# Performance work log

Hardware: AMD Instinct MI355X
Metric: run time of the kernel (lower is better)

Reference implementation:

```python
import jax, jax.numpy as jnp
import numpy as np

N_NODES = 100000
N_EDGES = 1600000


def gcn_conv(x, edge_index, W, b):
    # PyG GCNConv: add self-loops, symmetric degree normalization,
    # linear transform, scatter-sum aggregation, + bias.
    n = x.shape[0]
    loop = jnp.arange(n, dtype=edge_index.dtype)
    src = jnp.concatenate([edge_index[0], loop])
    dst = jnp.concatenate([edge_index[1], loop])
    deg = jnp.zeros((n,), x.dtype).at[dst].add(1.0)
    dinv = jnp.where(deg > 0, deg ** -0.5, 0.0)
    norm = dinv[src] * dinv[dst]            # [E+N]
    h = x @ W                               # [N, out]
    msg = h[src] * norm[:, None]            # gather + scale
    out = jax.ops.segment_sum(msg, dst, num_segments=n)
    return out + b


def setup_inputs() -> dict:
    key = jax.random.key(0)
    k1, k2, k3, k4 = jax.random.split(key, 4)
    d_in, d_lat, d_out = 512, 128, 64
    x = jax.random.normal(k1, (N_NODES, d_in), jnp.float32)
    edge_index = jax.random.randint(k2, (2, N_EDGES), 0, N_NODES, jnp.int64)
    W1 = jax.random.normal(k3, (d_in, d_lat), jnp.float32) * (d_in ** -0.5)
    b1 = jnp.zeros((d_lat,), jnp.float32)
    W2 = jax.random.normal(k4, (d_lat, d_out), jnp.float32) * (d_lat ** -0.5)
    b2 = jnp.zeros((d_out,), jnp.float32)
    return {"x": x, "edge_index": edge_index, "W1": W1, "b1": b1, "W2": W2, "b2": b2}


def reference(x, edge_index, W1, b1, W2, b2):
    h = gcn_conv(x, edge_index, W1, b1)
    h = gcn_conv(h, edge_index, W2, b2)
    return jax.nn.relu(h)
```

## Files before the change

kernel.cpp:

```cpp
#include <hip/hip_runtime.h>
#include <hip/hip_bf16.h>

typedef unsigned short u16;
typedef unsigned int   u32;

#define N_NODES 100000
#define N_EDGES 1600000

__device__ __forceinline__ float bf2f(u16 u) {
    union { u32 i; float f; } c; c.i = ((u32)u) << 16; return c.f;
}
__device__ __forceinline__ u16 f2bf(float f) {
    union { float f; u32 i; } c; c.f = f;
    u32 u = c.i;
    u += 0x7fffu + ((u >> 16) & 1u);
    return (u16)(u >> 16);
}

__global__ void k_detect(const u32* __restrict__ ei, int* __restrict__ flag) {
    if (threadIdx.x == 0 && blockIdx.x == 0) {
        u32 h = ei[1] | ei[3] | ei[5] | ei[7];
        *flag = (h == 0u) ? 1 : 0;
    }
}
__device__ __forceinline__ int edge_at(const u32* ei, int f, long pos) {
    return f ? (int)ei[2 * pos] : (int)ei[pos];
}


__global__ void k_degree(const u32* __restrict__ ei, const int* __restrict__ flag,
                         int* __restrict__ deg) {
    int e = blockIdx.x * blockDim.x + threadIdx.x;
    int f = *flag;
    if (e < N_EDGES) atomicAdd(&deg[edge_at(ei, f, (long)N_EDGES + e)], 1);
}

__global__ void k_scan_part(const int* __restrict__ deg, int* __restrict__ rowstart,
                            int* __restrict__ bsums) {
    __shared__ int sh[256];
    const int t = threadIdx.x, b = blockIdx.x;
    const int base = b * 2048 + t * 8;
    int v[8]; int s = 0;
#pragma unroll
    for (int i = 0; i < 8; i++) {
        int idx = base + i;
        v[i] = (idx < N_NODES) ? deg[idx] : 0;
        s += v[i];
    }
    sh[t] = s;
    __syncthreads();
    for (int d = 1; d < 256; d <<= 1) {
        int x = (t >= d) ? sh[t - d] : 0;
        __syncthreads();
        sh[t] += x;
        __syncthreads();
    }
    int acc = sh[t] - s;
#pragma unroll
    for (int i = 0; i < 8; i++) {
        int idx = base + i;
        if (idx < N_NODES) rowstart[idx] = acc;
        acc += v[i];
    }
    if (t == 255) bsums[b] = sh[255];
}

__global__ void k_scan_sums(const int* __restrict__ bsums, int* __restrict__ boffs, int nb) {
    if (threadIdx.x == 0 && blockIdx.x == 0) {
        int r = 0;
        for (int i = 0; i < nb; i++) { boffs[i] = r; r += bsums[i]; }
    }
}

__global__ void k_scan_add_dinv(int* __restrict__ rowstart, const int* __restrict__ boffs,
                                const int* __restrict__ deg, float* __restrict__ dinv) {
    int i = blockIdx.x * blockDim.x + threadIdx.x;
    if (i < N_NODES) {
        rowstart[i] += boffs[i >> 11];
        dinv[i] = rsqrtf((float)(deg[i] + 1));
    }
    if (i == 0) rowstart[N_NODES] = N_EDGES;
}

__global__ void k_fill(const u32* __restrict__ ei, const int* __restrict__ flag,
                       const int* __restrict__ rowstart, int* __restrict__ cursor,
                       int* __restrict__ csr) {
    int e = blockIdx.x * blockDim.x + threadIdx.x;
    int f = *flag;
    if (e < N_EDGES) {
        int s = edge_at(ei, f, e);
        int d = edge_at(ei, f, (long)N_EDGES + e);
        int p = rowstart[d] + atomicAdd(&cursor[d], 1);
        csr[p] = s;
    }
}


__global__ void k_w12(const float* __restrict__ W1, const float* __restrict__ W2,
                      float* __restrict__ W12f) {
    int idx = blockIdx.x * 256 + threadIdx.x;
    int k = idx >> 6, n = idx & 63;
    float acc = 0.f;
#pragma unroll 4
    for (int j = 0; j < 128; j++) acc += W1[k * 128 + j] * W2[j * 64 + n];
    W12f[idx] = acc;
}

__global__ void k_c1(const float* __restrict__ b1, const float* __restrict__ W2,
                     float* __restrict__ c1) {
    int n = threadIdx.x;
    float acc = 0.f;
    for (int j = 0; j < 128; j++) acc += b1[j] * W2[j * 64 + n];
    c1[n] = acc;
}

__global__ void k_fragB(const float* __restrict__ W12f, u16* __restrict__ Bt) {
    int idx = blockIdx.x * 256 + threadIdx.x;
    int l = idx & 63, c = (idx >> 6) & 3, kt = idx >> 8;
    int n = c * 16 + (l & 15);
    int k0 = kt * 32 + (l >> 4) * 8;
    u32 p[4];
#pragma unroll
    for (int j = 0; j < 4; j++) {
        u16 a = f2bf(W12f[(k0 + 2 * j) * 64 + n]);
        u16 b = f2bf(W12f[(k0 + 2 * j + 1) * 64 + n]);
        p[j] = (u32)a | ((u32)b << 16);
    }
    *(uint4*)&Bt[(long)idx * 8] = make_uint4(p[0], p[1], p[2], p[3]);
}


__global__ __launch_bounds__(256) void gemm_x(const float* __restrict__ A,
                                              const u16* __restrict__ Bt,
                                              u16* __restrict__ C, int M) {
    constexpr int SA = 40;
    __shared__ u16 As[128 * SA];
    typedef __attribute__((ext_vector_type(8))) short v8s;
    typedef __attribute__((ext_vector_type(4))) float v4f;

    const int t = threadIdx.x;
    const int wave = t >> 6, lane = t & 63;
    const int m = lane & 15, quad = lane >> 4;
    const int row0 = blockIdx.x * 128;

    v4f acc[2][4];
#pragma unroll
    for (int i = 0; i < 2; i++)
#pragma unroll
        for (int c = 0; c < 4; c++)
#pragma unroll
            for (int r = 0; r < 4; r++) acc[i][c][r] = 0.0f;

    const int arow = t >> 1, ahalf = t & 1;
    const long aoff = (long)(row0 + arow) * 512;
    const bool arow_ok = (row0 + arow) < M;

    for (int kt = 0; kt < 16; ++kt) {
        const int kk0 = kt * 32 + ahalf * 16;
        float4 f0 = make_float4(0.f, 0.f, 0.f, 0.f), f1 = f0, f2 = f0, f3 = f0;
        if (arow_ok) {
            f0 = *(const float4*)&A[aoff + kk0];
            f1 = *(const float4*)&A[aoff + kk0 + 4];
            f2 = *(const float4*)&A[aoff + kk0 + 8];
            f3 = *(const float4*)&A[aoff + kk0 + 12];
        }
        uint4 w0, w1;
        w0.x = (u32)f2bf(f0.x) | ((u32)f2bf(f0.y) << 16);
        w0.y = (u32)f2bf(f0.z) | ((u32)f2bf(f0.w) << 16);
        w0.z = (u32)f2bf(f1.x) | ((u32)f2bf(f1.y) << 16);
        w0.w = (u32)f2bf(f1.z) | ((u32)f2bf(f1.w) << 16);
        w1.x = (u32)f2bf(f2.x) | ((u32)f2bf(f2.y) << 16);
        w1.y = (u32)f2bf(f2.z) | ((u32)f2bf(f2.w) << 16);
        w1.z = (u32)f2bf(f3.x) | ((u32)f2bf(f3.y) << 16);
        w1.w = (u32)f2bf(f3.z) | ((u32)f2bf(f3.w) << 16);
        *(uint4*)&As[arow * SA + ahalf * 16] = w0;
        *(uint4*)&As[arow * SA + ahalf * 16 + 8] = w1;
        __syncthreads();
        v8s a0 = *(const v8s*)&As[(wave * 32 + m) * SA + quad * 8];
        v8s a1 = *(const v8s*)&As[(wave * 32 + 16 + m) * SA + quad * 8];
#pragma unroll
        for (int c = 0; c < 4; c++) {
            v8s b = *(const v8s*)&Bt[(long)((kt * 4 + c) * 64 + lane) * 8];
            acc[0][c] = __builtin_amdgcn_mfma_f32_16x16x32_bf16(a0, b, acc[0][c], 0, 0, 0);
            acc[1][c] = __builtin_amdgcn_mfma_f32_16x16x32_bf16(a1, b, acc[1][c], 0, 0, 0);
        }
        __syncthreads();
    }
#pragma unroll
    for (int i = 0; i < 2; i++)
#pragma unroll
        for (int c = 0; c < 4; c++)
#pragma unroll
            for (int r = 0; r < 4; r++) {
                int grow = row0 + wave * 32 + i * 16 + quad * 4 + r;
                if (grow < M) C[(long)grow * 64 + c * 16 + m] = f2bf(acc[i][c][r]);
            }
}


__global__ __launch_bounds__(256) void agg_a(const u16* __restrict__ z,
                                             const float* __restrict__ dinv,
                                             const int* __restrict__ rowstart,
                                             const int* __restrict__ csr,
                                             u16* __restrict__ y) {
    const int wave = threadIdx.x >> 6, lane = threadIdx.x & 63;
    const int n = blockIdx.x * 4 + wave;
    const int half = lane >> 5, l = lane & 31;
    const u32* z32 = (const u32*)z;
    float a0 = 0.f, a1 = 0.f;
    const float w0 = dinv[n];
    if (half == 0) {
        u32 d = z32[(long)n * 32 + l];
        float w = w0 * w0;
        a0 += bf2f((u16)(d & 0xffffu)) * w;
        a1 += bf2f((u16)(d >> 16)) * w;
    }
    const int i1 = rowstart[n + 1];
    for (int i = rowstart[n] + half; i < i1; i += 2) {
        int s = csr[i];
        float w = dinv[s] * w0;
        u32 d = z32[(long)s * 32 + l];
        a0 += bf2f((u16)(d & 0xffffu)) * w;
        a1 += bf2f((u16)(d >> 16)) * w;
    }
    a0 += __shfl_down(a0, 32);
    a1 += __shfl_down(a1, 32);
    if (half == 0) {
        u32 o = (u32)f2bf(a0) | ((u32)f2bf(a1) << 16);
        ((u32*)y)[(long)n * 32 + l] = o;
    }
}


__global__ __launch_bounds__(256) void agg_b(const u16* __restrict__ y,
                                             const float* __restrict__ dinv,
                                             const int* __restrict__ rowstart,
                                             const int* __restrict__ csr,
                                             const float* __restrict__ c1,
                                             const float* __restrict__ b2,
                                             float* __restrict__ out) {
    const int wave = threadIdx.x >> 6, lane = threadIdx.x & 63;
    const int n = blockIdx.x * 4 + wave;
    const int half = lane >> 5, l = lane & 31;
    const u32* y32 = (const u32*)y;
    float a0 = 0.f, a1 = 0.f, sacc = 0.f;
    const float w0 = dinv[n];
    if (half == 0) {
        u32 d = y32[(long)n * 32 + l];
        float w = w0 * w0;
        sacc += w;
        a0 += bf2f((u16)(d & 0xffffu)) * w;
        a1 += bf2f((u16)(d >> 16)) * w;
    }
    const int i1 = rowstart[n + 1];
    for (int i = rowstart[n] + half; i < i1; i += 2) {
        int s = csr[i];
        float w = dinv[s] * w0;
        sacc += w;
        u32 d = y32[(long)s * 32 + l];
        a0 += bf2f((u16)(d & 0xffffu)) * w;
        a1 += bf2f((u16)(d >> 16)) * w;
    }
    a0 += __shfl_down(a0, 32);
    a1 += __shfl_down(a1, 32);
    sacc += __shfl_down(sacc, 32);
    if (half == 0) {
        float2 cv = ((const float2*)c1)[l];
        float2 bv = ((const float2*)b2)[l];
        float r0 = fmaxf(a0 + sacc * cv.x + bv.x, 0.f);
        float r1 = fmaxf(a1 + sacc * cv.y + bv.y, 0.f);
        ((float2*)out)[(long)n * 32 + l] = make_float2(r0, r1);
    }
}


extern "C" void kernel_launch(void* const* d_in, const int* in_sizes, int n_in,
                              void* d_out, int out_size, void* d_ws, size_t ws_size,
                              hipStream_t stream) {
    const float* x  = (const float*)d_in[0];
    const u32*   ei = (const u32*)d_in[1];
    const float* W1 = (const float*)d_in[2];
    const float* b1 = (const float*)d_in[3];
    const float* W2 = (const float*)d_in[4];
    const float* b2 = (const float*)d_in[5];
    float* out = (float*)d_out;

    char* ws = (char*)d_ws;
    size_t o = 0;
    auto alloc = [&](size_t bytes) -> char* {
        char* p = ws + o;
        o = (o + bytes + 255) & ~(size_t)255;
        return p;
    };
    int*   deg      = (int*)  alloc(N_NODES * 4);
    float* dinv     = (float*)alloc(N_NODES * 4);
    int*   rowstart = (int*)  alloc((N_NODES + 1) * 4);
    int*   cursor   = (int*)  alloc(N_NODES * 4);
    int*   bsums    = (int*)  alloc(64 * 4);
    int*   boffs    = (int*)  alloc(64 * 4);
    int*   eflag    = (int*)  alloc(256);
    float* W12f     = (float*)alloc(512 * 64 * 4);
    u16*   Bt       = (u16*)  alloc(512 * 64 * 2);
    float* c1       = (float*)alloc(64 * 4);
    int*   csr      = (int*)  alloc((size_t)N_EDGES * 4);
    u16*   z        = (u16*)  alloc((size_t)N_NODES * 64 * 2);
    u16*   y        = (u16*)  alloc((size_t)N_NODES * 64 * 2);
    (void)ws_size;

    hipMemsetAsync(deg, 0, N_NODES * 4, stream);
    hipMemsetAsync(cursor, 0, N_NODES * 4, stream);

    const int EB = (N_EDGES + 255) / 256;
    const int NB = (N_NODES + 255) / 256;
    const int SCAN_BLKS = (N_NODES + 2047) / 2048;

    k_detect<<<1, 64, 0, stream>>>(ei, eflag);
    k_degree<<<EB, 256, 0, stream>>>(ei, eflag, deg);
    k_scan_part<<<SCAN_BLKS, 256, 0, stream>>>(deg, rowstart, bsums);
    k_scan_sums<<<1, 64, 0, stream>>>(bsums, boffs, SCAN_BLKS);
    k_scan_add_dinv<<<NB, 256, 0, stream>>>(rowstart, boffs, deg, dinv);
    k_fill<<<EB, 256, 0, stream>>>(ei, eflag, rowstart, cursor, csr);

    k_w12<<<128, 256, 0, stream>>>(W1, W2, W12f);
    k_c1<<<1, 64, 0, stream>>>(b1, W2, c1);
    k_fragB<<<16, 256, 0, stream>>>(W12f, Bt);

    gemm_x<<<(N_NODES + 127) / 128, 256, 0, stream>>>(x, Bt, z, N_NODES);
    agg_a<<<N_NODES / 4, 256, 0, stream>>>(z, dinv, rowstart, csr, y);
    agg_b<<<N_NODES / 4, 256, 0, stream>>>(y, dinv, rowstart, csr, c1, b2, out);
}
```

Before: 711.0 us.

## Prescale features by dinv, widen aggregation lanes, vectorize CSR build

The GEMM epilogue now multiplies each output row by dinv, so the aggregation loops become plain sums without a per-edge dinv multiply. The source-side normalisation for layer two is folded into a per-node factor (sfac) that agg_a precomputes. Both aggregation kernels now use four 16-lane groups reading 8 bytes each and unroll two edges per iteration, which raises memory-level parallelism. CSR construction handles four edges per thread with vector loads and initialises cursor directly from rowstart, removing a memset and a rowstart lookup. The extra bf16 rounding after prescaling slightly changes numerics.

```diff
diff --git a/kernel.cpp b/kernel.cpp
--- a/kernel.cpp
+++ b/kernel.cpp
@@ -16,6 +16,12 @@
     u += 0x7fffu + ((u >> 16) & 1u);
     return (u16)(u >> 16);
 }
+__device__ __forceinline__ void acc4(uint2 d, float& a0, float& a1, float& a2, float& a3) {
+    a0 += bf2f((u16)(d.x & 0xffffu));
+    a1 += bf2f((u16)(d.x >> 16));
+    a2 += bf2f((u16)(d.y & 0xffffu));
+    a3 += bf2f((u16)(d.y >> 16));
+}
 
 __global__ void k_detect(const u32* __restrict__ ei, int* __restrict__ flag) {
     if (threadIdx.x == 0 && blockIdx.x == 0) {
@@ -30,9 +36,24 @@
 
 __global__ void k_degree(const u32* __restrict__ ei, const int* __restrict__ flag,
                          int* __restrict__ deg) {
-    int e = blockIdx.x * blockDim.x + threadIdx.x;
+    int e4 = blockIdx.x * 256 + threadIdx.x;
     int f = *flag;
-    if (e < N_EDGES) atomicAdd(&deg[edge_at(ei, f, (long)N_EDGES + e)], 1);
+    long e = 4L * e4;
+    if (e + 3 < N_EDGES) {
+        int d0, d1, d2, d3;
+        if (f) {
+            uint4 a = *(const uint4*)&ei[2 * ((long)N_EDGES + e)];
+            uint4 b = *(const uint4*)&ei[2 * ((long)N_EDGES + e) + 4];
+            d0 = (int)a.x; d1 = (int)a.z; d2 = (int)b.x; d3 = (int)b.z;
+        } else {
+            uint4 a = *(const uint4*)&ei[(long)N_EDGES + e];
+            d0 = (int)a.x; d1 = (int)a.y; d2 = (int)a.z; d3 = (int)a.w;
+        }
+        atomicAdd(&deg[d0], 1); atomicAdd(&deg[d1], 1);
+        atomicAdd(&deg[d2], 1); atomicAdd(&deg[d3], 1);
+    } else {
+        for (; e < N_EDGES; e++) atomicAdd(&deg[edge_at(ei, f, (long)N_EDGES + e)], 1);
+    }
 }
 
 __global__ void k_scan_part(const int* __restrict__ deg, int* __restrict__ rowstart,
@@ -73,25 +94,48 @@
 }
 
 __global__ void k_scan_add_dinv(int* __restrict__ rowstart, const int* __restrict__ boffs,
-                                const int* __restrict__ deg, float* __restrict__ dinv) {
+                                const int* __restrict__ deg, float* __restrict__ dinv,
+                                int* __restrict__ cursor) {
     int i = blockIdx.x * blockDim.x + threadIdx.x;
     if (i < N_NODES) {
-        rowstart[i] += boffs[i >> 11];
+        int r = rowstart[i] + boffs[i >> 11];
+        rowstart[i] = r;
+        cursor[i] = r;
         dinv[i] = rsqrtf((float)(deg[i] + 1));
     }
     if (i == 0) rowstart[N_NODES] = N_EDGES;
 }
 
 __global__ void k_fill(const u32* __restrict__ ei, const int* __restrict__ flag,
-                       const int* __restrict__ rowstart, int* __restrict__ cursor,
-                       int* __restrict__ csr) {
-    int e = blockIdx.x * blockDim.x + threadIdx.x;
+                       int* __restrict__ cursor, int* __restrict__ csr) {
+    int e4 = blockIdx.x * 256 + threadIdx.x;
     int f = *flag;
-    if (e < N_EDGES) {
-        int s = edge_at(ei, f, e);
-        int d = edge_at(ei, f, (long)N_EDGES + e);
-        int p = rowstart[d] + atomicAdd(&cursor[d], 1);
-        csr[p] = s;
+    long e = 4L * e4;
+    if (e + 3 < N_EDGES) {
+        int s0, s1, s2, s3, d0, d1, d2, d3;
+        if (f) {
+            uint4 a = *(const uint4*)&ei[2 * e];
+            uint4 b = *(const uint4*)&ei[2 * e + 4];
+            s0 = (int)a.x; s1 = (int)a.z; s2 = (int)b.x; s3 = (int)b.z;
+            uint4 c = *(const uint4*)&ei[2 * ((long)N_EDGES + e)];
+            uint4 d = *(const uint4*)&ei[2 * ((long)N_EDGES + e) + 4];
+            d0 = (int)c.x; d1 = (int)c.z; d2 = (int)d.x; d3 = (int)d.z;
+        } else {
+            uint4 a = *(const uint4*)&ei[e];
+            s0 = (int)a.x; s1 = (int)a.y; s2 = (int)a.z; s3 = (int)a.w;
+            uint4 c = *(const uint4*)&ei[(long)N_EDGES + e];
+            d0 = (int)c.x; d1 = (int)c.y; d2 = (int)c.z; d3 = (int)c.w;
+        }
+        csr[atomicAdd(&cursor[d0], 1)] = s0;
+        csr[atomicAdd(&cursor[d1], 1)] = s1;
+        csr[atomicAdd(&cursor[d2], 1)] = s2;
+        csr[atomicAdd(&cursor[d3], 1)] = s3;
+    } else {
+        for (; e < N_EDGES; e++) {
+            int s = edge_at(ei, f, e);
+            int d = edge_at(ei, f, (long)N_EDGES + e);
+            csr[atomicAdd(&cursor[d], 1)] = s;
+        }
     }
 }
 
@@ -132,6 +176,7 @@
 
 __global__ __launch_bounds__(256) void gemm_x(const float* __restrict__ A,
                                               const u16* __restrict__ Bt,
+                                              const float* __restrict__ dinv,
                                               u16* __restrict__ C, int M) {
     constexpr int SA = 40;
     __shared__ u16 As[128 * SA];
@@ -189,87 +234,112 @@
 #pragma unroll
     for (int i = 0; i < 2; i++)
 #pragma unroll
-        for (int c = 0; c < 4; c++)
-#pragma unroll
-            for (int r = 0; r < 4; r++) {
-                int grow = row0 + wave * 32 + i * 16 + quad * 4 + r;
-                if (grow < M) C[(long)grow * 64 + c * 16 + m] = f2bf(acc[i][c][r]);
+        for (int r = 0; r < 4; r++) {
+            int grow = row0 + wave * 32 + i * 16 + quad * 4 + r;
+            if (grow < M) {
+                float w = dinv[grow];
+#pragma unroll
+                for (int c = 0; c < 4; c++)
+                    C[(long)grow * 64 + c * 16 + m] = f2bf(acc[i][c][r] * w);
             }
-}
-
-
-__global__ __launch_bounds__(256) void agg_a(const u16* __restrict__ z,
+        }
+}
+
+
+__global__ __launch_bounds__(256) void agg_a(const u16* __restrict__ zp,
                                              const float* __restrict__ dinv,
                                              const int* __restrict__ rowstart,
                                              const int* __restrict__ csr,
-                                             u16* __restrict__ y) {
+                                             u16* __restrict__ yp,
+                                             float* __restrict__ sfac) {
     const int wave = threadIdx.x >> 6, lane = threadIdx.x & 63;
     const int n = blockIdx.x * 4 + wave;
-    const int half = lane >> 5, l = lane & 31;
-    const u32* z32 = (const u32*)z;
-    float a0 = 0.f, a1 = 0.f;
+    const int g = lane >> 4, l = lane & 15;
+    const uint2* z2 = (const uint2*)zp;
+    float a0 = 0.f, a1 = 0.f, a2 = 0.f, a3 = 0.f, sd = 0.f;
     const float w0 = dinv[n];
-    if (half == 0) {
-        u32 d = z32[(long)n * 32 + l];
-        float w = w0 * w0;
-        a0 += bf2f((u16)(d & 0xffffu)) * w;
-        a1 += bf2f((u16)(d >> 16)) * w;
+    if (g == 0) {
+        uint2 d = z2[(long)n * 16 + l];
+        acc4(d, a0, a1, a2, a3);
+        sd = w0;
     }
     const int i1 = rowstart[n + 1];
-    for (int i = rowstart[n] + half; i < i1; i += 2) {
+    int i = rowstart[n] + g;
+    for (; i + 4 < i1; i += 8) {
+        int s0 = csr[i], s1 = csr[i + 4];
+        uint2 d0 = z2[(long)s0 * 16 + l];
+        uint2 d1 = z2[(long)s1 * 16 + l];
+        sd += dinv[s0] + dinv[s1];
+        acc4(d0, a0, a1, a2, a3);
+        acc4(d1, a0, a1, a2, a3);
+    }
+    if (i < i1) {
         int s = csr[i];
-        float w = dinv[s] * w0;
-        u32 d = z32[(long)s * 32 + l];
-        a0 += bf2f((u16)(d & 0xffffu)) * w;
-        a1 += bf2f((u16)(d >> 16)) * w;
-    }
-    a0 += __shfl_down(a0, 32);
-    a1 += __shfl_down(a1, 32);
-    if (half == 0) {
-        u32 o = (u32)f2bf(a0) | ((u32)f2bf(a1) << 16);
-        ((u32*)y)[(long)n * 32 + l] = o;
-    }
-}
-
-
-__global__ __launch_bounds__(256) void agg_b(const u16* __restrict__ y,
+        uint2 d = z2[(long)s * 16 + l];
+        sd += dinv[s];
+        acc4(d, a0, a1, a2, a3);
+    }
+    a0 += __shfl_xor(a0, 16); a0 += __shfl_xor(a0, 32);
+    a1 += __shfl_xor(a1, 16); a1 += __shfl_xor(a1, 32);
+    a2 += __shfl_xor(a2, 16); a2 += __shfl_xor(a2, 32);
+    a3 += __shfl_xor(a3, 16); a3 += __shfl_xor(a3, 32);
+    sd += __shfl_xor(sd, 16); sd += __shfl_xor(sd, 32);
+    if (g == 0) {
+        float w2 = w0 * w0;
+        uint2 o;
+        o.x = (u32)f2bf(a0 * w2) | ((u32)f2bf(a1 * w2) << 16);
+        o.y = (u32)f2bf(a2 * w2) | ((u32)f2bf(a3 * w2) << 16);
+        ((uint2*)yp)[(long)n * 16 + l] = o;
+        if (l == 0) sfac[n] = w0 * sd;
+    }
+}
+
+
+__global__ __launch_bounds__(256) void agg_b(const u16* __restrict__ yp,
                                              const float* __restrict__ dinv,
                                              const int* __restrict__ rowstart,
                                              const int* __restrict__ csr,
+                                             const float* __restrict__ sfac,
                                              const float* __restrict__ c1,
                                              const float* __restrict__ b2,
                                              float* __restrict__ out) {
     const int wave = threadIdx.x >> 6, lane = threadIdx.x & 63;
     const int n = blockIdx.x * 4 + wave;
-    const int half = lane >> 5, l = lane & 31;
-    const u32* y32 = (const u32*)y;
-    float a0 = 0.f, a1 = 0.f, sacc = 0.f;
-    const float w0 = dinv[n];
-    if (half == 0) {
-        u32 d = y32[(long)n * 32 + l];
-        float w = w0 * w0;
-        sacc += w;
-        a0 += bf2f((u16)(d & 0xffffu)) * w;
-        a1 += bf2f((u16)(d >> 16)) * w;
+    const int g = lane >> 4, l = lane & 15;
+    const uint2* y2 = (const uint2*)yp;
+    float a0 = 0.f, a1 = 0.f, a2 = 0.f, a3 = 0.f;
+    if (g == 0) {
+        uint2 d = y2[(long)n * 16 + l];
+        acc4(d, a0, a1, a2, a3);
     }
     const int i1 = rowstart[n + 1];
-    for (int i = rowstart[n] + half; i < i1; i += 2) {
-        int s = csr[i];
-        float w = dinv[s] * w0;
-        sacc += w;
-        u32 d = y32[(long)s * 32 + l];
-        a0 += bf2f((u16)(d & 0xffffu)) * w;
-        a1 += bf2f((u16)(d >> 16)) * w;
-    }
-    a0 += __shfl_down(a0, 32);
-    a1 += __shfl_down(a1, 32);
-    sacc += __shfl_down(sacc, 32);
-    if (half == 0) {
-        float2 cv = ((const float2*)c1)[l];
-        float2 bv = ((const float2*)b2)[l];
-        float r0 = fmaxf(a0 + sacc * cv.x + bv.x, 0.f);
-        float r1 = fmaxf(a1 + sacc * cv.y + bv.y, 0.f);
-        ((float2*)out)[(long)n * 32 + l] = make_float2(r0, r1);
+    int i = rowstart[n] + g;
+    for (; i + 4 < i1; i += 8) {
+        int s0 = csr[i], s1 = csr[i + 4];
+        uint2 d0 = y2[(long)s0 * 16 + l];
+        uint2 d1 = y2[(long)s1 * 16 + l];
+        acc4(d0, a0, a1, a2, a3);
+        acc4(d1, a0, a1, a2, a3);
+    }
+    if (i < i1) {
+        uint2 d = y2[(long)csr[i] * 16 + l];
+        acc4(d, a0, a1, a2, a3);
+    }
+    a0 += __shfl_xor(a0, 16); a0 += __shfl_xor(a0, 32);
+    a1 += __shfl_xor(a1, 16); a1 += __shfl_xor(a1, 32);
+    a2 += __shfl_xor(a2, 16); a2 += __shfl_xor(a2, 32);
+    a3 += __shfl_xor(a3, 16); a3 += __shfl_xor(a3, 32);
+    if (g == 0) {
+        const float w0 = dinv[n];
+        const float sn = sfac[n];
+        float4 cv = ((const float4*)c1)[l];
+        float4 bv = ((const float4*)b2)[l];
+        float4 r;
+        r.x = fmaxf(a0 * w0 + sn * cv.x + bv.x, 0.f);
+        r.y = fmaxf(a1 * w0 + sn * cv.y + bv.y, 0.f);
+        r.z = fmaxf(a2 * w0 + sn * cv.z + bv.z, 0.f);
+        r.w = fmaxf(a3 * w0 + sn * cv.w + bv.w, 0.f);
+        ((float4*)out)[(long)n * 16 + l] = r;
     }
 }
 
@@ -302,30 +372,30 @@
     float* W12f     = (float*)alloc(512 * 64 * 4);
     u16*   Bt       = (u16*)  alloc(512 * 64 * 2);
     float* c1       = (float*)alloc(64 * 4);
+    float* sfac     = (float*)alloc(N_NODES * 4);
     int*   csr      = (int*)  alloc((size_t)N_EDGES * 4);
     u16*   z        = (u16*)  alloc((size_t)N_NODES * 64 * 2);
     u16*   y        = (u16*)  alloc((size_t)N_NODES * 64 * 2);
     (void)ws_size;
 
     hipMemsetAsync(deg, 0, N_NODES * 4, stream);
-    hipMemsetAsync(cursor, 0, N_NODES * 4, stream);
-
-    const int EB = (N_EDGES + 255) / 256;
+
     const int NB = (N_NODES + 255) / 256;
+    const int EB4 = (N_EDGES / 4 + 255) / 256;
     const int SCAN_BLKS = (N_NODES + 2047) / 2048;
 
     k_detect<<<1, 64, 0, stream>>>(ei, eflag);
-    k_degree<<<EB, 256, 0, stream>>>(ei, eflag, deg);
+    k_degree<<<EB4, 256, 0, stream>>>(ei, eflag, deg);
     k_scan_part<<<SCAN_BLKS, 256, 0, stream>>>(deg, rowstart, bsums);
     k_scan_sums<<<1, 64, 0, stream>>>(bsums, boffs, SCAN_BLKS);
-    k_scan_add_dinv<<<NB, 256, 0, stream>>>(rowstart, boffs, deg, dinv);
-    k_fill<<<EB, 256, 0, stream>>>(ei, eflag, rowstart, cursor, csr);
+    k_scan_add_dinv<<<NB, 256, 0, stream>>>(rowstart, boffs, deg, dinv, cursor);
+    k_fill<<<EB4, 256, 0, stream>>>(ei, eflag, cursor, csr);
 
     k_w12<<<128, 256, 0, stream>>>(W1, W2, W12f);
     k_c1<<<1, 64, 0, stream>>>(b1, W2, c1);
     k_fragB<<<16, 256, 0, stream>>>(W12f, Bt);
 
-    gemm_x<<<(N_NODES + 127) / 128, 256, 0, stream>>>(x, Bt, z, N_NODES);
-    agg_a<<<N_NODES / 4, 256, 0, stream>>>(z, dinv, rowstart, csr, y);
-    agg_b<<<N_NODES / 4, 256, 0, stream>>>(y, dinv, rowstart, csr, c1, b2, out);
-}
+    gemm_x<<<(N_NODES + 127) / 128, 256, 0, stream>>>(x, Bt, dinv, z, N_NODES);
+    agg_a<<<N_NODES / 4, 256, 0, stream>>>(z, dinv, rowstart, csr, y, sfac);
+    agg_b<<<N_NODES / 4, 256, 0, stream>>>(y, dinv, rowstart, csr, sfac, c1, b2, out);
+}
```

Measured after the change: 615.5 us. 13.4% less time.
